# Kernel tuning notes

Hardware: AMD Instinct MI355X
Metric: run time of the kernel (lower is better)

The kernel has to match this reference:

```python
import jax, jax.numpy as jnp
import numpy as np

B, S, D, DIM = 8, 4096, 1024, 512  # batch, src nodes, dst nodes, feature dim


def setup_inputs() -> dict:
    key = jax.random.key(0)
    k1, k2, k3, k4, k5 = jax.random.split(key, 5)
    scale = 1.0 / np.sqrt(DIM)
    return {
        "src_val": jax.random.normal(k1, (B, S, DIM), dtype=jnp.float32),
        "src_state": jax.random.normal(k2, (B, S), dtype=jnp.float32),
        "dst_val": jax.random.normal(k3, (B, D, DIM), dtype=jnp.float32),
        "W_route": jax.random.normal(k4, (DIM, DIM), dtype=jnp.float32) * scale,
        "W_val": jax.random.normal(k5, (DIM, DIM), dtype=jnp.float32) * scale,
    }


def reference(src_val, src_state, dst_val, W_route, W_val):
    # Pairwise route logits: bilinear bipartite attention, [B, S, D]
    inv_sqrt_d = 1.0 / jnp.sqrt(jnp.asarray(src_val.shape[-1], src_val.dtype))
    q = jnp.einsum("bsd,de->bse", src_val, W_route)
    logits = jnp.einsum("bse,bke->bsk", q, dst_val) * inv_sqrt_d
    # route compression: softmax over dst nodes (dim=-1)
    routes = jax.nn.softmax(logits, axis=-1)
    # projections
    projected_val = jnp.einsum("bsd,de->bse", src_val, W_val)  # [B, S, DIM]
    projected_state = src_state                                 # identity state proj, [B, S]
    sender_strength = jax.nn.softplus(src_state)                # [B, S]
    # weighted routing + accumulation
    weighted_routes = routes * sender_strength[..., None]       # [B, S, D]
    delta_state = jnp.einsum("bsk,bs->bk", weighted_routes, projected_state)   # [B, D]
    delta_val = jnp.einsum("bsk,bsd->bkd", weighted_routes, projected_val)     # [B, D, DIM]
    return delta_state, delta_val
```

## Files before the change

kernel.cpp:

```cpp
#include <hip/hip_runtime.h>
#include <hip/hip_fp16.h>

#define B_   8
#define S_   4096
#define DD_  1024
#define DIM_ 512
#define SCALE 0.044194173824159216f

typedef __bf16 bf16x8 __attribute__((ext_vector_type(8)));
typedef float  floatx4 __attribute__((ext_vector_type(4)));

__device__ inline unsigned short f2bf(float f) {
    union { float f; unsigned int u; } v; v.f = f;
    unsigned int r = v.u + 0x7fffu + ((v.u >> 16) & 1u);
    return (unsigned short)(r >> 16);
}
__device__ inline float bf2f(unsigned short h) {
    union { unsigned int u; float f; } v; v.u = ((unsigned int)h) << 16;
    return v.f;
}
__device__ inline uint4 cvt8(const float* __restrict__ g) {
    float4 f0 = *(const float4*)g;
    float4 f1 = *(const float4*)(g + 4);
    unsigned short tmp[8] = {f2bf(f0.x), f2bf(f0.y), f2bf(f0.z), f2bf(f0.w),
                             f2bf(f1.x), f2bf(f1.y), f2bf(f1.z), f2bf(f1.w)};
    return *(const uint4*)tmp;
}
__device__ inline void async16(unsigned short* lds, const unsigned short* g) {
    __builtin_amdgcn_global_load_lds(
        (const __attribute__((address_space(1))) void*)g,
        (__attribute__((address_space(3))) void*)lds, 16, 0, 0);
}

template <int AF32, int BF32>
__device__ inline void mainloop(unsigned short* As, unsigned short* Bs,
                                const void* Ap, size_t lda,
                                const void* Bp, size_t ldb,
                                int kIters, floatx4 (&acc)[4][4]) {
    const int t = threadIdx.x, lane = t & 63, wave = t >> 6;
    const int rA = t >> 2;
    const int cA = ((t & 3) ^ ((t >> 3) & 3)) * 8;
    const int mrow = (wave >> 1) * 64, ncol = (wave & 1) * 64;
    const int fr = lane & 15, fk = (lane >> 4) * 8;
    const int swz = (((fk >> 3) ^ ((fr >> 1) & 3)) << 3);

    const unsigned short* gA16 = nullptr; const float* gA32 = nullptr;
    const unsigned short* gB16 = nullptr; const float* gB32 = nullptr;
    if (AF32) gA32 = (const float*)Ap + (size_t)rA * lda + cA;
    else      gA16 = (const unsigned short*)Ap + (size_t)rA * lda + cA;
    if (BF32) gB32 = (const float*)Bp + (size_t)rA * ldb + cA;
    else      gB16 = (const unsigned short*)Bp + (size_t)rA * ldb + cA;

    unsigned short* ldsA = As + wave * 512;
    unsigned short* ldsB = Bs + wave * 512;

    auto stage = [&](int buf) {
        const int o = buf * 4096;
        if (AF32) {
            *(uint4*)&As[o + t * 8]        = cvt8(gA32);
            *(uint4*)&As[o + 2048 + t * 8] = cvt8(gA32 + 64 * lda);
            gA32 += 32;
        } else {
            async16(ldsA + o,        gA16);
            async16(ldsA + o + 2048, gA16 + 64 * lda);
            gA16 += 32;
        }
        if (BF32) {
            *(uint4*)&Bs[o + t * 8]        = cvt8(gB32);
            *(uint4*)&Bs[o + 2048 + t * 8] = cvt8(gB32 + 64 * ldb);
            gB32 += 32;
        } else {
            async16(ldsB + o,        gB16);
            async16(ldsB + o + 2048, gB16 + 64 * ldb);
            gB16 += 32;
        }
    };

    stage(0);
    __syncthreads();
    for (int kt = 0; kt < kIters; ++kt) {
        if (kt + 1 < kIters) stage((kt + 1) & 1);
        const int cur = (kt & 1) * 4096;
        bf16x8 af[4], bfr[4];
#pragma unroll
        for (int i = 0; i < 4; ++i)
            af[i] = *(const bf16x8*)&As[cur + (mrow + i * 16 + fr) * 32 + swz];
#pragma unroll
        for (int j = 0; j < 4; ++j)
            bfr[j] = *(const bf16x8*)&Bs[cur + (ncol + j * 16 + fr) * 32 + swz];
#pragma unroll
        for (int i = 0; i < 4; ++i)
#pragma unroll
            for (int j = 0; j < 4; ++j)
                acc[i][j] = __builtin_amdgcn_mfma_f32_16x16x32_bf16(af[i], bfr[j],
                                                                    acc[i][j], 0, 0, 0);
        __syncthreads();
    }
}

#define EPILOGUE_COORDS                                     \
    const int lane = threadIdx.x & 63, wave = threadIdx.x >> 6; \
    const int mrow = (wave >> 1) * 64, ncol = (wave & 1) * 64;  \
    const int col = lane & 15, q = lane >> 4;

#define ACC_INIT                                            \
    floatx4 acc[4][4];                                      \
    _Pragma("unroll") for (int i = 0; i < 4; ++i)           \
        _Pragma("unroll") for (int j = 0; j < 4; ++j)       \
            acc[i][j] = (floatx4){0.f, 0.f, 0.f, 0.f};

__global__ __launch_bounds__(256) void k_prep(const float* __restrict__ src,
                                              unsigned short* __restrict__ srcb) {
    const size_t idx = ((size_t)blockIdx.x * 256 + threadIdx.x) * 8;
    *(uint4*)&srcb[idx] = cvt8(src + idx);
}

__global__ __launch_bounds__(256) void k_dstWr(const float* __restrict__ dst,
                                               const float* __restrict__ Wr,
                                               unsigned short* __restrict__ DW) {
    __shared__ unsigned short As[2 * 128 * 32];
    __shared__ unsigned short Bs[2 * 128 * 32];
    const int n0 = blockIdx.x * 128, m0 = blockIdx.y * 128;
    ACC_INIT
    mainloop<1, 1>(As, Bs, dst + (size_t)m0 * DIM_, DIM_,
                   Wr + (size_t)n0 * DIM_, DIM_, DIM_ / 32, acc);
    EPILOGUE_COORDS
#pragma unroll
    for (int i = 0; i < 4; ++i)
#pragma unroll
        for (int j = 0; j < 4; ++j)
#pragma unroll
            for (int r = 0; r < 4; ++r)
                DW[(size_t)(m0 + mrow + i * 16 + q * 4 + r) * DIM_ +
                   n0 + ncol + j * 16 + col] = f2bf(acc[i][j][r] * SCALE);
}

__global__ __launch_bounds__(256) void k_logitsT(const unsigned short* __restrict__ DW,
                                                 const unsigned short* __restrict__ srcb,
                                                 unsigned short* __restrict__ LTb,
                                                 float* __restrict__ Lpart) {
    __shared__ unsigned short As[2 * 128 * 32];
    __shared__ unsigned short Bs[2 * 128 * 32];
    __shared__ float csum[8][128];
    const int n = blockIdx.x;
    const int b = n & 7;
    const int rem = n >> 3;
    const int xs = rem >> 3;
    const int yd = rem & 7;
    const int n0 = xs * 128, m0 = yd * 128;
    ACC_INIT
    mainloop<0, 0>(As, Bs,
                   DW + (size_t)b * DD_ * DIM_ + (size_t)m0 * DIM_, DIM_,
                   srcb + (size_t)b * S_ * DIM_ + (size_t)n0 * DIM_, DIM_,
                   DIM_ / 32, acc);
    EPILOGUE_COORDS
    unsigned short* LT = LTb + (size_t)b * DD_ * S_;
    float psum[4] = {0.f, 0.f, 0.f, 0.f};
#pragma unroll
    for (int i = 0; i < 4; ++i)
#pragma unroll
        for (int j = 0; j < 4; ++j)
#pragma unroll
            for (int r = 0; r < 4; ++r) {
                float e = __expf(acc[i][j][r]);
                LT[(size_t)(m0 + mrow + i * 16 + q * 4 + r) * S_ +
                   n0 + ncol + j * 16 + col] = f2bf(e);
                psum[j] += e;
            }
    const int slice = (wave >> 1) * 4 + q;
#pragma unroll
    for (int j = 0; j < 4; ++j) csum[slice][ncol + j * 16 + col] = psum[j];
    __syncthreads();
    const int t = threadIdx.x;
    if (t < 128) {
        float v = 0.f;
#pragma unroll
        for (int k = 0; k < 8; ++k) v += csum[k][t];
        Lpart[((size_t)b * 8 + yd) * S_ + n0 + t] = v;
    }
}

__global__ __launch_bounds__(256) void k_finalize(const float* __restrict__ state,
                                                  const float* __restrict__ Lpart,
                                                  float* __restrict__ scale) {
    const int i = blockIdx.x * 256 + threadIdx.x;
    const int b = i >> 12, s = i & (S_ - 1);
    float d = 0.f;
#pragma unroll
    for (int k = 0; k < 8; ++k) d += Lpart[((size_t)b * 8 + k) * S_ + s];
    const float st = state[i];
    const float sp = (st > 15.f) ? st : log1pf(__expf(st));
    scale[i] = sp / d;
}

__global__ __launch_bounds__(256) void k_srcT(const unsigned short* __restrict__ srcb,
                                              const float* __restrict__ scale,
                                              unsigned short* __restrict__ srcST) {
    __shared__ unsigned short Ts[64 * 65];
    const int s0 = blockIdx.x * 64, d0 = blockIdx.y * 64, b = blockIdx.z;
    const int t = threadIdx.x;
    {
        const int r = t >> 2, c0 = (t & 3) * 16;
        const unsigned short* g =
            srcb + (size_t)b * S_ * DIM_ + (size_t)(s0 + r) * DIM_ + d0 + c0;
        uint4 v0 = *(const uint4*)g;
        uint4 v1 = *(const uint4*)(g + 8);
        const unsigned short* e0 = (const unsigned short*)&v0;
        const unsigned short* e1 = (const unsigned short*)&v1;
        const float sc = scale[(size_t)b * S_ + s0 + r];
#pragma unroll
        for (int i = 0; i < 8; ++i) {
            Ts[r * 65 + c0 + i]     = f2bf(bf2f(e0[i]) * sc);
            Ts[r * 65 + c0 + 8 + i] = f2bf(bf2f(e1[i]) * sc);
        }
    }
    __syncthreads();
    {
        const int rr = t >> 2, c0 = (t & 3) * 16;
        unsigned short tmp[16];
#pragma unroll
        for (int j = 0; j < 16; ++j) tmp[j] = Ts[(c0 + j) * 65 + rr];
        unsigned short* o =
            srcST + (size_t)b * DIM_ * S_ + (size_t)(d0 + rr) * S_ + s0 + c0;
        *(uint4*)o = *(const uint4*)tmp;
        *(uint4*)(o + 8) = *(const uint4*)(tmp + 8);
    }
}

__global__ __launch_bounds__(256) void k_dstate(const unsigned short* __restrict__ LT,
                                                const float* __restrict__ state,
                                                const float* __restrict__ scale,
                                                float* __restrict__ out) {
    const int b = blockIdx.y;
    const int dd = blockIdx.x * 4 + (threadIdx.x >> 6);
    const int lane = threadIdx.x & 63;
    const unsigned short* row = LT + (size_t)b * DD_ * S_ + (size_t)dd * S_;
    const float* st = state + (size_t)b * S_;
    const float* sc = scale + (size_t)b * S_;

    float acc = 0.f;
#pragma unroll
    for (int it = 0; it < S_ / 512; ++it) {
        const int s = it * 512 + lane * 8;
        uint4 v = *(const uint4*)(row + s);
        const unsigned short* e = (const unsigned short*)&v;
        float4 f0 = *(const float4*)(st + s);
        float4 f1 = *(const float4*)(st + s + 4);
        float4 c0 = *(const float4*)(sc + s);
        float4 c1 = *(const float4*)(sc + s + 4);
        acc += bf2f(e[0]) * f0.x * c0.x + bf2f(e[1]) * f0.y * c0.y +
               bf2f(e[2]) * f0.z * c0.z + bf2f(e[3]) * f0.w * c0.w +
               bf2f(e[4]) * f1.x * c1.x + bf2f(e[5]) * f1.y * c1.y +
               bf2f(e[6]) * f1.z * c1.z + bf2f(e[7]) * f1.w * c1.w;
    }
#pragma unroll
    for (int off = 32; off; off >>= 1) acc += __shfl_down(acc, off);
    if (lane == 0) out[(size_t)b * DD_ + dd] = acc;
}

__global__ __launch_bounds__(256) void k_dU(const unsigned short* __restrict__ LTb,
                                            const unsigned short* __restrict__ srcST,
                                            __half* __restrict__ Pp) {
    __shared__ unsigned short As[2 * 128 * 32];
    __shared__ unsigned short Bs[2 * 128 * 32];
    const int n = blockIdx.x;
    const int z = (n & 7) + 8 * (n >> 8);
    const int rem = (n >> 3) & 31;
    const int xe = rem >> 3;
    const int yd = rem & 7;
    const int b = z >> 2, ks = z & 3;
    const int n0 = xe * 128, m0 = yd * 128;
    ACC_INIT
    mainloop<0, 0>(As, Bs,
                   LTb + (size_t)b * DD_ * S_ + (size_t)m0 * S_ + ks * 1024, S_,
                   srcST + (size_t)b * DIM_ * S_ + (size_t)n0 * S_ + ks * 1024, S_,
                   1024 / 32, acc);
    EPILOGUE_COORDS
    __half* O = Pp + (size_t)ks * B_ * DD_ * DIM_ + (size_t)b * DD_ * DIM_;
#pragma unroll
    for (int i = 0; i < 4; ++i)
#pragma unroll
        for (int j = 0; j < 4; ++j)
#pragma unroll
            for (int r = 0; r < 4; ++r)
                O[(size_t)(m0 + mrow + i * 16 + q * 4 + r) * DIM_ +
                  n0 + ncol + j * 16 + col] = __float2half(acc[i][j][r]);
}

__global__ __launch_bounds__(256) void k_reduceU(const __half* __restrict__ Pp,
                                                 unsigned short* __restrict__ U,
                                                 const float* __restrict__ Wv,
                                                 unsigned short* __restrict__ WvT) {
    __shared__ float Ts[64 * 68];
    const int t = threadIdx.x;
    if (blockIdx.x < 2048) {
        const size_t idx = ((size_t)blockIdx.x * 256 + t) * 8;
        const size_t n = (size_t)B_ * DD_ * DIM_;
        float o[8] = {0.f, 0.f, 0.f, 0.f, 0.f, 0.f, 0.f, 0.f};
#pragma unroll
        for (int ks = 0; ks < 4; ++ks) {
            uint4 v = *(const uint4*)(Pp + (size_t)ks * n + idx);
            const __half* h = (const __half*)&v;
#pragma unroll
            for (int j = 0; j < 8; ++j) o[j] += __half2float(h[j]);
        }
        unsigned short tmp[8];
#pragma unroll
        for (int j = 0; j < 8; ++j) tmp[j] = f2bf(o[j]);
        *(uint4*)&U[idx] = *(const uint4*)tmp;
        return;
    }
    const int n2 = blockIdx.x - 2048;
    const int d0 = (n2 & 7) * 64, e0 = (n2 >> 3) * 64;
    {
        const int r = t >> 2, c0 = (t & 3) * 16;
        const float* g = Wv + (size_t)(d0 + r) * DIM_ + e0 + c0;
#pragma unroll
        for (int i = 0; i < 4; ++i)
            *(float4*)&Ts[r * 68 + c0 + i * 4] = *(const float4*)(g + i * 4);
    }
    __syncthreads();
    {
        const int rr = t >> 2, c0 = (t & 3) * 16;
        unsigned short tmp[16];
#pragma unroll
        for (int j = 0; j < 16; ++j) tmp[j] = f2bf(Ts[(c0 + j) * 68 + rr]);
        unsigned short* o = WvT + (size_t)(e0 + rr) * DIM_ + d0 + c0;
        *(uint4*)o = *(const uint4*)tmp;
        *(uint4*)(o + 8) = *(const uint4*)(tmp + 8);
    }
}

__global__ __launch_bounds__(256) void k_dvalW(const unsigned short* __restrict__ U,
                                               const unsigned short* __restrict__ WvT,
                                               float* __restrict__ d_val) {
    __shared__ unsigned short As[2 * 128 * 32];
    __shared__ unsigned short Bs[2 * 128 * 32];
    const int n0 = blockIdx.x * 128, m0 = blockIdx.y * 128;
    ACC_INIT
    mainloop<0, 0>(As, Bs, U + (size_t)m0 * DIM_, DIM_,
                   WvT + (size_t)n0 * DIM_, DIM_, DIM_ / 32, acc);
    EPILOGUE_COORDS
#pragma unroll
    for (int i = 0; i < 4; ++i)
#pragma unroll
        for (int j = 0; j < 4; ++j)
#pragma unroll
            for (int r = 0; r < 4; ++r)
                d_val[(size_t)(m0 + mrow + i * 16 + q * 4 + r) * DIM_ +
                      n0 + ncol + j * 16 + col] = acc[i][j][r];
}

extern "C" void kernel_launch(void* const* d_in, const int* in_sizes, int n_in,
                              void* d_out, int out_size, void* d_ws, size_t ws_size,
                              hipStream_t stream) {
    const float* src   = (const float*)d_in[0];
    const float* state = (const float*)d_in[1];
    const float* dst   = (const float*)d_in[2];
    const float* Wr    = (const float*)d_in[3];
    const float* Wv    = (const float*)d_in[4];

    unsigned short* srcb = (unsigned short*)d_ws;
    __half* Pp = (__half*)d_ws;
    unsigned short* LT = srcb + (size_t)B_ * S_ * DIM_;
    unsigned short* U  = LT;
    unsigned short* WvT = U + (size_t)B_ * DD_ * DIM_;
    unsigned short* C = LT + (size_t)B_ * DD_ * S_;
    unsigned short* DW = C;
    float* Lpart = (float*)(DW + (size_t)B_ * DD_ * DIM_);
    unsigned short* srcST = C;

    float* d_state = (float*)d_out;
    float* d_val   = (float*)d_out + B_ * DD_;
    float* scale   = d_val;

    k_prep<<<dim3(8192), 256, 0, stream>>>(src, srcb);
    k_dstWr<<<dim3(DIM_ / 128, (B_ * DD_) / 128), 256, 0, stream>>>(dst, Wr, DW);
    k_logitsT<<<dim3(2048), 256, 0, stream>>>(DW, srcb, LT, Lpart);
    k_finalize<<<dim3((B_ * S_) / 256), 256, 0, stream>>>(state, Lpart, scale);
    k_dstate<<<dim3(DD_ / 4, B_), 256, 0, stream>>>(LT, state, scale, d_state);
    k_srcT<<<dim3(S_ / 64, DIM_ / 64, B_), 256, 0, stream>>>(srcb, scale, srcST);
    k_dU<<<dim3(1024), 256, 0, stream>>>(LT, srcST, Pp);
    k_reduceU<<<dim3(2048 + 64), 256, 0, stream>>>(Pp, U, Wv, WvT);
    k_dvalW<<<dim3(DIM_ / 128, (B_ * DD_) / 128), 256, 0, stream>>>(U, WvT, d_val);
}
```

Measured before the change: 289.4 us.

## Use 256x256 tiles with 8-wave pipelined mainloop for logits and dU GEMMs

```diff
diff --git a/kernel.cpp b/kernel.cpp
--- a/kernel.cpp
+++ b/kernel.cpp
@@ -31,6 +31,123 @@
         (const __attribute__((address_space(1))) void*)g,
         (__attribute__((address_space(3))) void*)lds, 16, 0, 0);
 }
+
+__device__ inline void vwait8() { asm volatile("s_waitcnt vmcnt(8)" ::: "memory"); }
+__device__ inline void vwait4() { asm volatile("s_waitcnt vmcnt(4)" ::: "memory"); }
+__device__ inline void vwait0() { asm volatile("s_waitcnt vmcnt(0)" ::: "memory"); }
+#define SBAR   __builtin_amdgcn_s_barrier()
+#define SCHED0 __builtin_amdgcn_sched_barrier(0)
+
+__device__ inline void mainloop256(unsigned short* As, unsigned short* Bs,
+                                   const unsigned short* __restrict__ Ap, size_t lda,
+                                   const unsigned short* __restrict__ Bp, size_t ldb,
+                                   int nk, floatx4 (&acc)[8][4]) {
+    const int t = threadIdx.x, lane = t & 63, w = t >> 6;
+    const int wm = w >> 2, wn = w & 3;
+    const int fr = lane & 15;
+    const int swz  = (((lane >> 4) ^ ((fr >> 1) & 3)) << 3);
+    const int csrc = (((t & 3) ^ ((t >> 3) & 3)) << 3);
+
+    const unsigned short* gA = Ap + (size_t)(t >> 2) * lda + csrc;
+    const unsigned short* gB = Bp + (size_t)(t >> 2) * ldb + csrc;
+    unsigned short* ldsA = As + w * 512;
+    unsigned short* ldsB = Bs + w * 512;
+
+    auto stgA = [&](int buf, int kt, int kh) {
+        const unsigned short* g = gA + (size_t)kt * 64 + kh * 32;
+        async16(ldsA + buf * 16384 + kh * 8192,        g);
+        async16(ldsA + buf * 16384 + kh * 8192 + 4096, g + (size_t)128 * lda);
+    };
+    auto stgB = [&](int buf, int kt, int kh) {
+        const unsigned short* g = gB + (size_t)kt * 64 + kh * 32;
+        async16(ldsB + buf * 16384 + kh * 8192,        g);
+        async16(ldsB + buf * 16384 + kh * 8192 + 4096, g + (size_t)128 * ldb);
+    };
+
+    stgA(0, 0, 0); stgB(0, 0, 0); stgA(0, 0, 1); stgB(0, 0, 1);
+    stgA(1, 1, 0); stgB(1, 1, 0);
+    vwait8();
+    SCHED0;
+    SBAR;
+
+    const int arow = wm * 128 + fr, brow = wn * 64 + fr;
+    for (int kt = 0; kt < nk; ++kt) {
+        const int cur = kt & 1;
+        const bool sA = kt + 1 < nk, sB = kt + 2 < nk;
+        const int base = cur * 16384;
+        bf16x8 a[4], b[4], a2[4];
+#pragma unroll
+        for (int i = 0; i < 4; ++i)
+            a[i] = *(const bf16x8*)&As[base + (arow + i * 16) * 32 + swz];
+#pragma unroll
+        for (int j = 0; j < 4; ++j)
+            b[j] = *(const bf16x8*)&Bs[base + (brow + j * 16) * 32 + swz];
+        if (sA) stgA(cur ^ 1, kt + 1, 1);
+        SCHED0;
+        SBAR;
+        __builtin_amdgcn_s_setprio(1);
+#pragma unroll
+        for (int i = 0; i < 4; ++i)
+#pragma unroll
+            for (int j = 0; j < 4; ++j)
+                acc[i][j] = __builtin_amdgcn_mfma_f32_16x16x32_bf16(a[i], b[j], acc[i][j], 0, 0, 0);
+        __builtin_amdgcn_s_setprio(0);
+        SBAR;
+#pragma unroll
+        for (int i = 0; i < 4; ++i)
+            a2[i] = *(const bf16x8*)&As[base + (arow + 64 + i * 16) * 32 + swz];
+        if (sA) stgB(cur ^ 1, kt + 1, 1);
+        SCHED0;
+        SBAR;
+        __builtin_amdgcn_s_setprio(1);
+#pragma unroll
+        for (int i = 0; i < 4; ++i)
+#pragma unroll
+            for (int j = 0; j < 4; ++j)
+                acc[4 + i][j] = __builtin_amdgcn_mfma_f32_16x16x32_bf16(a2[i], b[j], acc[4 + i][j], 0, 0, 0);
+        __builtin_amdgcn_s_setprio(0);
+        if (sA) vwait8(); else vwait0();
+        SBAR;
+#pragma unroll
+        for (int i = 0; i < 4; ++i)
+            a[i] = *(const bf16x8*)&As[base + 8192 + (arow + i * 16) * 32 + swz];
+#pragma unroll
+        for (int j = 0; j < 4; ++j)
+            b[j] = *(const bf16x8*)&Bs[base + 8192 + (brow + j * 16) * 32 + swz];
+        if (sB) stgA(cur, kt + 2, 0);
+        SCHED0;
+        SBAR;
+        __builtin_amdgcn_s_setprio(1);
+#pragma unroll
+        for (int i = 0; i < 4; ++i)
+#pragma unroll
+            for (int j = 0; j < 4; ++j)
+                acc[i][j] = __builtin_amdgcn_mfma_f32_16x16x32_bf16(a[i], b[j], acc[i][j], 0, 0, 0);
+        __builtin_amdgcn_s_setprio(0);
+        SBAR;
+#pragma unroll
+        for (int i = 0; i < 4; ++i)
+            a2[i] = *(const bf16x8*)&As[base + 8192 + (arow + 64 + i * 16) * 32 + swz];
+        if (sB) stgB(cur, kt + 2, 0);
+        SCHED0;
+        SBAR;
+        __builtin_amdgcn_s_setprio(1);
+#pragma unroll
+        for (int i = 0; i < 4; ++i)
+#pragma unroll
+            for (int j = 0; j < 4; ++j)
+                acc[4 + i][j] = __builtin_amdgcn_mfma_f32_16x16x32_bf16(a2[i], b[j], acc[4 + i][j], 0, 0, 0);
+        __builtin_amdgcn_s_setprio(0);
+        if (sA) { if (sB) vwait8(); else vwait4(); }
+        SBAR;
+    }
+}
+
+#define ACC_INIT8                                           \
+    floatx4 acc[8][4];                                      \
+    _Pragma("unroll") for (int i = 0; i < 8; ++i)           \
+        _Pragma("unroll") for (int j = 0; j < 4; ++j)       \
+            acc[i][j] = (floatx4){0.f, 0.f, 0.f, 0.f};
 
 template <int AF32, int BF32>
 __device__ inline void mainloop(unsigned short* As, unsigned short* Bs,
@@ -135,48 +252,51 @@
                    n0 + ncol + j * 16 + col] = f2bf(acc[i][j][r] * SCALE);
 }
 
-__global__ __launch_bounds__(256) void k_logitsT(const unsigned short* __restrict__ DW,
+__global__ __launch_bounds__(512) void k_logitsT(const unsigned short* __restrict__ DW,
                                                  const unsigned short* __restrict__ srcb,
                                                  unsigned short* __restrict__ LTb,
                                                  float* __restrict__ Lpart) {
-    __shared__ unsigned short As[2 * 128 * 32];
-    __shared__ unsigned short Bs[2 * 128 * 32];
-    __shared__ float csum[8][128];
+    __shared__ __align__(16) unsigned short As[32768];
+    __shared__ __align__(16) unsigned short Bs[32768];
     const int n = blockIdx.x;
     const int b = n & 7;
     const int rem = n >> 3;
-    const int xs = rem >> 3;
-    const int yd = rem & 7;
-    const int n0 = xs * 128, m0 = yd * 128;
-    ACC_INIT
-    mainloop<0, 0>(As, Bs,
-                   DW + (size_t)b * DD_ * DIM_ + (size_t)m0 * DIM_, DIM_,
-                   srcb + (size_t)b * S_ * DIM_ + (size_t)n0 * DIM_, DIM_,
-                   DIM_ / 32, acc);
-    EPILOGUE_COORDS
+    const int xs = rem >> 2;
+    const int yd = rem & 3;
+    const int n0 = xs * 256, m0 = yd * 256;
+    ACC_INIT8
+    mainloop256(As, Bs,
+                DW + (size_t)b * DD_ * DIM_ + (size_t)m0 * DIM_, DIM_,
+                srcb + (size_t)b * S_ * DIM_ + (size_t)n0 * DIM_, DIM_,
+                DIM_ / 64, acc);
+    const int t = threadIdx.x, lane = t & 63, w = t >> 6;
+    const int wm = w >> 2, wn = w & 3;
+    const int c16 = lane & 15, q = lane >> 4;
+    const int row0 = m0 + wm * 128, col0 = n0 + wn * 64;
     unsigned short* LT = LTb + (size_t)b * DD_ * S_;
     float psum[4] = {0.f, 0.f, 0.f, 0.f};
 #pragma unroll
-    for (int i = 0; i < 4; ++i)
+    for (int i = 0; i < 8; ++i)
 #pragma unroll
         for (int j = 0; j < 4; ++j)
 #pragma unroll
             for (int r = 0; r < 4; ++r) {
                 float e = __expf(acc[i][j][r]);
-                LT[(size_t)(m0 + mrow + i * 16 + q * 4 + r) * S_ +
-                   n0 + ncol + j * 16 + col] = f2bf(e);
+                LT[(size_t)(row0 + i * 16 + q * 4 + r) * S_ +
+                   col0 + j * 16 + c16] = f2bf(e);
                 psum[j] += e;
             }
-    const int slice = (wave >> 1) * 4 + q;
-#pragma unroll
-    for (int j = 0; j < 4; ++j) csum[slice][ncol + j * 16 + col] = psum[j];
+    float* csum = (float*)As;
+    const int slice = wm * 4 + q;
+#pragma unroll
+    for (int j = 0; j < 4; ++j)
+        csum[slice * 256 + wn * 64 + j * 16 + c16] = psum[j];
     __syncthreads();
-    const int t = threadIdx.x;
-    if (t < 128) {
+    if (t < 256) {
         float v = 0.f;
 #pragma unroll
-        for (int k = 0; k < 8; ++k) v += csum[k][t];
-        Lpart[((size_t)b * 8 + yd) * S_ + n0 + t] = v;
+        for (int k = 0; k < 8; ++k) v += csum[k * 256 + t];
+        Lpart[((size_t)b * 4 + yd) * S_ + n0 + t] = v;
     }
 }
 
@@ -187,7 +307,7 @@
     const int b = i >> 12, s = i & (S_ - 1);
     float d = 0.f;
 #pragma unroll
-    for (int k = 0; k < 8; ++k) d += Lpart[((size_t)b * 8 + k) * S_ + s];
+    for (int k = 0; k < 4; ++k) d += Lpart[((size_t)b * 4 + k) * S_ + s];
     const float st = state[i];
     const float sp = (st > 15.f) ? st : log1pf(__expf(st));
     scale[i] = sp / d;
@@ -258,33 +378,37 @@
     if (lane == 0) out[(size_t)b * DD_ + dd] = acc;
 }
 
-__global__ __launch_bounds__(256) void k_dU(const unsigned short* __restrict__ LTb,
+__global__ __launch_bounds__(512) void k_dU(const unsigned short* __restrict__ LTb,
                                             const unsigned short* __restrict__ srcST,
                                             __half* __restrict__ Pp) {
-    __shared__ unsigned short As[2 * 128 * 32];
-    __shared__ unsigned short Bs[2 * 128 * 32];
+    __shared__ __align__(16) unsigned short As[32768];
+    __shared__ __align__(16) unsigned short Bs[32768];
     const int n = blockIdx.x;
-    const int z = (n & 7) + 8 * (n >> 8);
-    const int rem = (n >> 3) & 31;
-    const int xe = rem >> 3;
-    const int yd = rem & 7;
+    const int qn = n >> 3;
+    const int tile = qn & 7, zhi = qn >> 3;
+    const int z = (n & 7) + 8 * zhi;
     const int b = z >> 2, ks = z & 3;
-    const int n0 = xe * 128, m0 = yd * 128;
-    ACC_INIT
-    mainloop<0, 0>(As, Bs,
-                   LTb + (size_t)b * DD_ * S_ + (size_t)m0 * S_ + ks * 1024, S_,
-                   srcST + (size_t)b * DIM_ * S_ + (size_t)n0 * S_ + ks * 1024, S_,
-                   1024 / 32, acc);
-    EPILOGUE_COORDS
+    const int xe = tile >> 2;
+    const int yd = tile & 3;
+    const int n0 = xe * 256, m0 = yd * 256;
+    ACC_INIT8
+    mainloop256(As, Bs,
+                LTb + (size_t)b * DD_ * S_ + (size_t)m0 * S_ + ks * 1024, S_,
+                srcST + (size_t)b * DIM_ * S_ + (size_t)n0 * S_ + ks * 1024, S_,
+                1024 / 64, acc);
+    const int t = threadIdx.x, lane = t & 63, w = t >> 6;
+    const int wm = w >> 2, wn = w & 3;
+    const int c16 = lane & 15, q = lane >> 4;
+    const int row0 = m0 + wm * 128, col0 = n0 + wn * 64;
     __half* O = Pp + (size_t)ks * B_ * DD_ * DIM_ + (size_t)b * DD_ * DIM_;
 #pragma unroll
-    for (int i = 0; i < 4; ++i)
+    for (int i = 0; i < 8; ++i)
 #pragma unroll
         for (int j = 0; j < 4; ++j)
 #pragma unroll
             for (int r = 0; r < 4; ++r)
-                O[(size_t)(m0 + mrow + i * 16 + q * 4 + r) * DIM_ +
-                  n0 + ncol + j * 16 + col] = __float2half(acc[i][j][r]);
+                O[(size_t)(row0 + i * 16 + q * 4 + r) * DIM_ +
+                  col0 + j * 16 + c16] = __float2half(acc[i][j][r]);
 }
 
 __global__ __launch_bounds__(256) void k_reduceU(const __half* __restrict__ Pp,
@@ -376,11 +500,11 @@
 
     k_prep<<<dim3(8192), 256, 0, stream>>>(src, srcb);
     k_dstWr<<<dim3(DIM_ / 128, (B_ * DD_) / 128), 256, 0, stream>>>(dst, Wr, DW);
-    k_logitsT<<<dim3(2048), 256, 0, stream>>>(DW, srcb, LT, Lpart);
+    k_logitsT<<<dim3(512), 512, 0, stream>>>(DW, srcb, LT, Lpart);
     k_finalize<<<dim3((B_ * S_) / 256), 256, 0, stream>>>(state, Lpart, scale);
     k_dstate<<<dim3(DD_ / 4, B_), 256, 0, stream>>>(LT, state, scale, d_state);
     k_srcT<<<dim3(S_ / 64, DIM_ / 64, B_), 256, 0, stream>>>(srcb, scale, srcST);
-    k_dU<<<dim3(1024), 256, 0, stream>>>(LT, srcST, Pp);
+    k_dU<<<dim3(256), 512, 0, stream>>>(LT, srcST, Pp);
     k_reduceU<<<dim3(2048 + 64), 256, 0, stream>>>(Pp, U, Wv, WvT);
     k_dvalW<<<dim3(DIM_ / 128, (B_ * DD_) / 128), 256, 0, stream>>>(U, WvT, d_val);
 }
```

After: 278.9 us. 1.04x faster.
